# Performance work log

Hardware: AMD Instinct MI355X
Metric: run time of the kernel (lower is better)

## Reference

```python
import jax, jax.numpy as jnp
import numpy as np

DIM = 64
NUM_GRAPHS = 256
SLOPE = 11.0 / 48.0  # RReLU eval slope = ((1/8)+(1/3))/2
EPS = 1e-5


def _bn(x, g, b):
    m = x.mean(0)
    v = x.var(0)  # biased, matches torch BN normalization
    return (x - m) * jax.lax.rsqrt(v + EPS) * g + b


def _rrelu(x):
    return jnp.where(x >= 0, x, SLOPE * x)


def _gru(x, h, Wih, Whh, bih, bhh):
    gi = x @ Wih.T + bih
    gh = h @ Whh.T + bhh
    ir, iz, inn = jnp.split(gi, 3, -1)
    hr, hz, hn = jnp.split(gh, 3, -1)
    r = jax.nn.sigmoid(ir + hr)
    z = jax.nn.sigmoid(iz + hz)
    n = jnp.tanh(inn + r * hn)
    return (1.0 - z) * n + z * h


def _nnconv(x, ei, We, bias, n_nodes):
    # edge-conditioned conv: gather src, per-edge matmul, scatter-mean to dst
    src, dst = ei[0], ei[1]
    msg = jnp.einsum('ei,eio->eo', x[src], We)
    s = jax.ops.segment_sum(msg, dst, num_segments=n_nodes)
    cnt = jax.ops.segment_sum(jnp.ones((ei.shape[1],), x.dtype), dst, num_segments=n_nodes)
    return s / jnp.maximum(cnt, 1.0)[:, None] + bias


def _seg_softmax(e, seg, nseg):
    m = jax.ops.segment_max(e, seg, num_segments=nseg)
    ex = jnp.exp(e - m[seg])
    den = jax.ops.segment_sum(ex, seg, num_segments=nseg)
    return ex / den[seg]


def _set2set(x, seg, nseg, Wih, Whh, bih, bhh, steps=3):
    H = x.shape[-1]
    q_star = jnp.zeros((nseg, 2 * H), x.dtype)
    h = jnp.zeros((nseg, H), x.dtype)
    c = jnp.zeros((nseg, H), x.dtype)
    for _ in range(steps):
        gates = q_star @ Wih.T + bih + h @ Whh.T + bhh
        i, f, g, o = jnp.split(gates, 4, -1)
        c = jax.nn.sigmoid(f) * c + jax.nn.sigmoid(i) * jnp.tanh(g)
        h = jax.nn.sigmoid(o) * jnp.tanh(c)
        e = jnp.sum(x * h[seg], -1)
        a = _seg_softmax(e, seg, nseg)
        r = jax.ops.segment_sum(a[:, None] * x, seg, num_segments=nseg)
        q_star = jnp.concatenate([h, r], -1)
    return q_star


def reference(x, edge_index, edge_attr, edge_index3, edge_attr3, batch,
              bnx_g, bnx_b, Wn, bnode, We, be, Wnn1, bias1,
              Wih1, Whh1, bih1, bhh1, bnc_g, bnc_b, Wc1, bc1, Wc2, bc2,
              Wnn2, bias2, Wih2, Whh2, bih2, bhh2,
              Ws_ih, Ws_hh, bs_ih, bs_hh, bno_g, bno_b, Ww, Wb):
    N = x.shape[0]
    out = _rrelu(_bn(x, bnx_g, bnx_b) @ Wn + bnode)          # [N, 64]
    ea = _rrelu(edge_attr @ We + be)                          # [E, 12]
    W1 = (ea @ Wnn1).reshape(-1, DIM, DIM)                    # [E, 64, 64]
    h = out
    for _ in range(2):
        m = _rrelu(_nnconv(out, edge_index, W1, bias1, N))
        h = _gru(m, h, Wih1, Whh1, bih1, bhh1)
        out = h
    out = _bn(out, bnc_g, bnc_b)
    out = _rrelu(out @ Wc1 + bc1)
    out = _rrelu(out @ Wc2 + bc2)                             # [N, 128] (dropout=identity in eval)
    ei3s = jnp.concatenate([edge_index3, edge_index3[::-1]], axis=1)
    ea3s = jnp.concatenate([edge_attr3, edge_attr3], axis=0)
    W2 = (ea3s @ Wnn2).reshape(-1, 2 * DIM, 2 * DIM)          # [2*E3, 128, 128]
    h = out
    for _ in range(2):
        m = _rrelu(_nnconv(out, ei3s, W2, bias2, N))
        h = _gru(m, h, Wih2, Whh2, bih2, bhh2)
        out = h
    cbi = batch[edge_index3[0]]
    pool = _set2set(out, batch, NUM_GRAPHS, Ws_ih, Ws_hh, bs_ih, bs_hh)[cbi]
    t0 = out[edge_index3[0]]
    t1 = out[edge_index3[1]]
    yhat = jnp.concatenate([(t0 + t1) * 0.5, t0 * t1, (t0 - t1) ** 2, pool], axis=1)  # [E3, 640]
    yhat = _bn(yhat, bno_g, bno_b)
    w = edge_attr3 @ Ww
    b = edge_attr3 @ Wb
    return jnp.sum(yhat * w, axis=1) + b[:, 0]


def setup_inputs() -> dict:
    key = jax.random.key(0)
    ks = iter(jax.random.split(key, 64))
    def nrm(shape, scale=1.0):
        return jax.random.normal(next(ks), shape, jnp.float32) * scale
    def lin(i, o):
        return nrm((i, o), 1.0 / np.sqrt(i))
    N, E, E3 = 8192, 16384, 1024
    inp = {}
    inp['x'] = nrm((N, 8))
    inp['edge_index'] = jax.random.randint(next(ks), (2, E), 0, N)
    inp['edge_attr'] = nrm((E, 19))
    inp['edge_index3'] = jax.random.randint(next(ks), (2, E3), 0, N)
    inp['edge_attr3'] = nrm((E3, 8))
    inp['batch'] = jnp.repeat(jnp.arange(NUM_GRAPHS), N // NUM_GRAPHS)
    inp['bnx_g'] = jnp.ones(8); inp['bnx_b'] = jnp.zeros(8)
    inp['Wn'] = lin(8, 64); inp['bnode'] = jnp.zeros(64)
    inp['We'] = lin(19, 12); inp['be'] = jnp.zeros(12)
    inp['Wnn1'] = lin(12, DIM * DIM) * 0.5; inp['bias1'] = jnp.zeros(64)
    inp['Wih1'] = nrm((192, 64), 1.0 / np.sqrt(64)); inp['Whh1'] = nrm((192, 64), 1.0 / np.sqrt(64))
    inp['bih1'] = jnp.zeros(192); inp['bhh1'] = jnp.zeros(192)
    inp['bnc_g'] = jnp.ones(64); inp['bnc_b'] = jnp.zeros(64)
    inp['Wc1'] = lin(64, 128); inp['bc1'] = jnp.zeros(128)
    inp['Wc2'] = lin(128, 128); inp['bc2'] = jnp.zeros(128)
    inp['Wnn2'] = lin(8, 4 * DIM * DIM) * 0.5; inp['bias2'] = jnp.zeros(128)
    inp['Wih2'] = nrm((384, 128), 1.0 / np.sqrt(128)); inp['Whh2'] = nrm((384, 128), 1.0 / np.sqrt(128))
    inp['bih2'] = jnp.zeros(384); inp['bhh2'] = jnp.zeros(384)
    inp['Ws_ih'] = nrm((512, 256), 1.0 / np.sqrt(256)); inp['Ws_hh'] = nrm((512, 128), 1.0 / np.sqrt(128))
    inp['bs_ih'] = jnp.zeros(512); inp['bs_hh'] = jnp.zeros(512)
    inp['bno_g'] = jnp.ones(640); inp['bno_b'] = jnp.zeros(640)
    inp['Ww'] = lin(8, 640); inp['Wb'] = lin(8, 1)
    return inp
```

## Files before the change

### kernel.cpp

```cpp
#include <hip/hip_runtime.h>
#include <hip/hip_bf16.h>
#include <math.h>

#define N_NODES 8192
#define N_EDGES 16384
#define N_E3    1024
#define NGRAPH  256
#define NPG     32
#define SLOPE   (11.0f/48.0f)
#define BN_EPS  1e-5f

__device__ __forceinline__ float rrelu(float v){ return v >= 0.f ? v : SLOPE*v; }
__device__ __forceinline__ float sigm(float v){ return 1.f/(1.f+__expf(-v)); }

typedef _Float16 f16;
typedef __attribute__((ext_vector_type(8))) _Float16 half8v;
typedef __attribute__((ext_vector_type(4))) float f32x4;

__device__ __forceinline__ void zero_tail(int zb, float* zptr, int zcount) {
  float4 z4 = make_float4(0.f,0.f,0.f,0.f);
  int bd = blockDim.x;
  for (int i = zb*bd + (int)threadIdx.x; i*4 < zcount; i += 16*bd)
    ((float4*)zptr)[i] = z4;
}

__global__ __launch_bounds__(256) void conv1f_k(const float* __restrict__ nodeA,
    const int* __restrict__ ei, const float* __restrict__ ea,
    const f16* __restrict__ Wz1h, float* __restrict__ sbuf) {
  int t = threadIdx.x, lane = t & 63, wv = t >> 6;
  int e0 = blockIdx.x*64 + wv*16;
  int eA = e0 + (lane & 15);
  int src = ei[eA];
  int kb0 = (lane >> 4) * 8;
  const float* ap = nodeA + (size_t)src*64 + kb0;
  float4 v0 = *(const float4*)ap,      v1 = *(const float4*)(ap+4);
  float4 v2 = *(const float4*)(ap+32), v3 = *(const float4*)(ap+36);
  half8v a0, a1;
  a0[0]=(f16)v0.x; a0[1]=(f16)v0.y; a0[2]=(f16)v0.z; a0[3]=(f16)v0.w;
  a0[4]=(f16)v1.x; a0[5]=(f16)v1.y; a0[6]=(f16)v1.z; a0[7]=(f16)v1.w;
  a1[0]=(f16)v2.x; a1[1]=(f16)v2.y; a1[2]=(f16)v2.z; a1[3]=(f16)v2.w;
  a1[4]=(f16)v3.x; a1[5]=(f16)v3.y; a1[6]=(f16)v3.z; a1[7]=(f16)v3.w;
  float eav[12];
  #pragma unroll
  for (int kg = 0; kg < 12; kg++) eav[kg] = ea[eA*12 + kg];

  f32x4 acc[4] = {{0,0,0,0},{0,0,0,0},{0,0,0,0},{0,0,0,0}};
  #pragma unroll
  for (int kg = 0; kg < 12; kg++) {
    f16 s = (f16)eav[kg];
    half8v s0, s1;
    #pragma unroll
    for (int u = 0; u < 8; u++) { s0[u] = a0[u]*s; s1[u] = a1[u]*s; }
    #pragma unroll
    for (int jf = 0; jf < 4; jf++) {
      const f16* wp = Wz1h + (size_t)(kg*64 + jf*16 + (lane & 15))*64 + kb0;
      acc[jf] = __builtin_amdgcn_mfma_f32_16x16x32_f16(s0, *(const half8v*)wp, acc[jf], 0, 0, 0);
      acc[jf] = __builtin_amdgcn_mfma_f32_16x16x32_f16(s1, *(const half8v*)(wp+32), acc[jf], 0, 0, 0);
    }
  }
  int dstv[4];
  #pragma unroll
  for (int r = 0; r < 4; r++) dstv[r] = ei[N_EDGES + e0 + ((lane>>4)<<2) + r];
  #pragma unroll
  for (int jf = 0; jf < 4; jf++) {
    int col = jf*16 + (lane & 15);
    #pragma unroll
    for (int r = 0; r < 4; r++)
      atomicAdd(&sbuf[dstv[r]*64 + col], acc[jf][r]);
  }
}

__global__ __launch_bounds__(512) void conv2f_k(const float* __restrict__ nodeB,
    const int* __restrict__ ei3, const float* __restrict__ ea3,
    const f16* __restrict__ W2fh, float* __restrict__ sbuf) {
  int t = threadIdx.x, lane = t & 63, wv = t >> 6;
  int eg = blockIdx.x >> 1, qh = blockIdx.x & 1;
  int kgh = wv >> 2, jp = wv & 3;
  int e0 = eg * 16;
  int eA = e0 + (lane & 15);
  int src = ei3[eA];
  int kb0 = qh*64 + (lane >> 4) * 8;
  const float* ap = nodeB + (size_t)src*128 + kb0;
  half8v a0, a1;
  {
    float4 w0 = *(const float4*)ap,        w1 = *(const float4*)(ap+4);
    float4 w2 = *(const float4*)(ap + 32), w3 = *(const float4*)(ap+36);
    a0[0]=(f16)w0.x; a0[1]=(f16)w0.y; a0[2]=(f16)w0.z; a0[3]=(f16)w0.w;
    a0[4]=(f16)w1.x; a0[5]=(f16)w1.y; a0[6]=(f16)w1.z; a0[7]=(f16)w1.w;
    a1[0]=(f16)w2.x; a1[1]=(f16)w2.y; a1[2]=(f16)w2.z; a1[3]=(f16)w2.w;
    a1[4]=(f16)w3.x; a1[5]=(f16)w3.y; a1[6]=(f16)w3.z; a1[7]=(f16)w3.w;
  }
  int eb = eA & (N_E3 - 1);
  float eav[4];
  #pragma unroll
  for (int kk = 0; kk < 4; kk++) eav[kk] = ea3[eb*8 + kgh*4 + kk];

  f32x4 acc[2] = {{0,0,0,0},{0,0,0,0}};
  #pragma unroll
  for (int kk = 0; kk < 4; kk++) {
    f16 s = (f16)eav[kk];
    half8v s0, s1;
    #pragma unroll
    for (int u = 0; u < 8; u++) { s0[u] = a0[u]*s; s1[u] = a1[u]*s; }
    int kg = kgh*4 + kk;
    #pragma unroll
    for (int jj = 0; jj < 2; jj++) {
      int jf = jp*2 + jj;
      const f16* wp = W2fh + (size_t)(kg*128 + jf*16 + (lane & 15))*128 + kb0;
      acc[jj] = __builtin_amdgcn_mfma_f32_16x16x32_f16(s0, *(const half8v*)wp, acc[jj], 0, 0, 0);
      acc[jj] = __builtin_amdgcn_mfma_f32_16x16x32_f16(s1, *(const half8v*)(wp+32), acc[jj], 0, 0, 0);
    }
  }
  int dstv[4];
  #pragma unroll
  for (int r = 0; r < 4; r++) dstv[r] = ei3[(e0 + ((lane>>4)<<2) + r + N_E3) & (2*N_E3 - 1)];
  #pragma unroll
  for (int jj = 0; jj < 2; jj++) {
    int col = (jp*2+jj)*16 + (lane & 15);
    #pragma unroll
    for (int r = 0; r < 4; r++)
      atomicAdd(&sbuf[dstv[r]*128 + col], acc[jj][r]);
  }
}

template<int LOGH, int STATS>
__global__ void gruf_k(const float* __restrict__ sbuf, const float* __restrict__ cnt,
                       const float* __restrict__ mbias,
                       const f16* __restrict__ Wih, const f16* __restrict__ Whh,
                       const float* __restrict__ bih, const float* __restrict__ bhh,
                       const float* __restrict__ hold, float* __restrict__ hnew,
                       float* __restrict__ bns1, float* __restrict__ bns2,
                       int nblk, float* __restrict__ zptr, int zcount) {
  if ((int)blockIdx.x >= nblk) { zero_tail(blockIdx.x - nblk, zptr, zcount); return; }
  const int H = 1 << LOGH;
  const int K = H;
  const int jt = H >> 6;
  int t = threadIdx.x;
  int lane = t & 63, wv = t >> 6;
  int wpb = blockDim.x >> 6;
  int bm = blockIdx.x / jt, bj = blockIdx.x % jt;
  int n0 = bm * (wpb << 4) + (wv << 4);
  int j0 = bj << 6;
  int row = n0 + (lane & 15);
  int kb0 = (lane >> 4) * 8;

  f32x4 aR[4]  = {{0,0,0,0},{0,0,0,0},{0,0,0,0},{0,0,0,0}};
  f32x4 aZ[4]  = {{0,0,0,0},{0,0,0,0},{0,0,0,0},{0,0,0,0}};
  f32x4 aIN[4] = {{0,0,0,0},{0,0,0,0},{0,0,0,0},{0,0,0,0}};
  f32x4 aHN[4] = {{0,0,0,0},{0,0,0,0},{0,0,0,0},{0,0,0,0}};

  float dn = 1.f / fmaxf(cnt[row], 1.0f);
  for (int k0 = 0; k0 < K; k0 += 32) {
    int kb = k0 + kb0;
    const float* ap = sbuf + (size_t)row * K + kb;
    float4 v0 = *(const float4*)ap, v1 = *(const float4*)(ap + 4);
    float4 b0 = *(const float4*)(mbias + kb), b1 = *(const float4*)(mbias + kb + 4);
    half8v af;
    af[0]=(f16)rrelu(v0.x*dn+b0.x); af[1]=(f16)rrelu(v0.y*dn+b0.y);
    af[2]=(f16)rrelu(v0.z*dn+b0.z); af[3]=(f16)rrelu(v0.w*dn+b0.w);
    af[4]=(f16)rrelu(v1.x*dn+b1.x); af[5]=(f16)rrelu(v1.y*dn+b1.y);
    af[6]=(f16)rrelu(v1.z*dn+b1.z); af[7]=(f16)rrelu(v1.w*dn+b1.w);
    #pragma unroll
    for (int jf = 0; jf < 4; jf++) {
      int wr = j0 + jf*16 + (lane & 15);
      half8v wR = *(const half8v*)(Wih + (size_t)wr*K + kb);
      half8v wZ = *(const half8v*)(Wih + (size_t)(H + wr)*K + kb);
      half8v wN = *(const half8v*)(Wih + (size_t)(2*H + wr)*K + kb);
      aR[jf]  = __builtin_amdgcn_mfma_f32_16x16x32_f16(af, wR, aR[jf], 0, 0, 0);
      aZ[jf]  = __builtin_amdgcn_mfma_f32_16x16x32_f16(af, wZ, aZ[jf], 0, 0, 0);
      aIN[jf] = __builtin_amdgcn_mfma_f32_16x16x32_f16(af, wN, aIN[jf], 0, 0, 0);
    }
  }
  for (int k0 = 0; k0 < K; k0 += 32) {
    int kb = k0 + kb0;
    const float* ap = hold + (size_t)row * K + kb;
    float4 v0 = *(const float4*)ap, v1 = *(const float4*)(ap + 4);
    half8v af;
    af[0]=(f16)v0.x; af[1]=(f16)v0.y; af[2]=(f16)v0.z; af[3]=(f16)v0.w;
    af[4]=(f16)v1.x; af[5]=(f16)v1.y; af[6]=(f16)v1.z; af[7]=(f16)v1.w;
    #pragma unroll
    for (int jf = 0; jf < 4; jf++) {
      int wr = j0 + jf*16 + (lane & 15);
      half8v wR = *(const half8v*)(Whh + (size_t)wr*K + kb);
      half8v wZ = *(const half8v*)(Whh + (size_t)(H + wr)*K + kb);
      half8v wN = *(const half8v*)(Whh + (size_t)(2*H + wr)*K + kb);
      aR[jf]  = __builtin_amdgcn_mfma_f32_16x16x32_f16(af, wR, aR[jf], 0, 0, 0);
      aZ[jf]  = __builtin_amdgcn_mfma_f32_16x16x32_f16(af, wZ, aZ[jf], 0, 0, 0);
      aHN[jf] = __builtin_amdgcn_mfma_f32_16x16x32_f16(af, wN, aHN[jf], 0, 0, 0);
    }
  }
  int r0 = n0 + ((lane >> 4) << 2);
  #pragma unroll
  for (int jf = 0; jf < 4; jf++) {
    int col = j0 + jf*16 + (lane & 15);
    float bR = bih[col] + bhh[col];
    float bZ = bih[H + col] + bhh[H + col];
    float bI = bih[2*H + col], bH = bhh[2*H + col];
    float ssum = 0.f, sq = 0.f;
    #pragma unroll
    for (int r = 0; r < 4; r++) {
      float rr = sigm(aR[jf][r] + bR);
      float zz = sigm(aZ[jf][r] + bZ);
      float nn = tanhf(aIN[jf][r] + bI + rr*(aHN[jf][r] + bH));
      float ho = hold[(size_t)(r0 + r)*H + col];
      float hv = (1.f - zz)*nn + zz*ho;
      hnew[(size_t)(r0 + r)*H + col] = hv;
      if (STATS) { ssum += hv; sq += hv*hv; }
    }
    if (STATS) {
      ssum += __shfl_xor(ssum, 16); ssum += __shfl_xor(ssum, 32);
      sq   += __shfl_xor(sq, 16);   sq   += __shfl_xor(sq, 32);
      if (lane < 16) { atomicAdd(&bns1[col], ssum); atomicAdd(&bns2[col], sq); }
    }
  }
}

__global__ __launch_bounds__(256) void fcf_k(const float* __restrict__ A,
    const f16* __restrict__ W1, const float* __restrict__ b1v,
    const f16* __restrict__ W2, const float* __restrict__ b2v,
    const float* __restrict__ bns1, const float* __restrict__ bns2,
    const float* __restrict__ g, const float* __restrict__ b,
    float* __restrict__ outB,
    int nblk, float* __restrict__ zptr, int zcount) {
  if ((int)blockIdx.x >= nblk) { zero_tail(blockIdx.x - nblk, zptr, zcount); return; }
  __shared__ f16 y1s[4][16][128];
  int t = threadIdx.x, lane = t & 63, wv = t >> 6;
  int n0 = blockIdx.x*64 + wv*16;
  int row = n0 + (lane & 15);
  int kb0 = (lane >> 4) * 8;
  const float invN = 1.f / (float)N_NODES;

  const float* ap = A + (size_t)row*64 + kb0;
  half8v af0, af1;
  #pragma unroll
  for (int u = 0; u < 8; u++) {
    int k0i = kb0 + u, k1i = 32 + kb0 + u;
    float m0 = bns1[k0i]*invN, m1 = bns1[k1i]*invN;
    float va0 = bns2[k0i]*invN - m0*m0, va1 = bns2[k1i]*invN - m1*m1;
    af0[u] = (f16)((ap[u]    - m0)*rsqrtf(va0+BN_EPS)*g[k0i] + b[k0i]);
    af1[u] = (f16)((ap[32+u] - m1)*rsqrtf(va1+BN_EPS)*g[k1i] + b[k1i]);
  }
  f32x4 acc1[8] = {{0,0,0,0},{0,0,0,0},{0,0,0,0},{0,0,0,0},
                   {0,0,0,0},{0,0,0,0},{0,0,0,0},{0,0,0,0}};
  #pragma unroll
  for (int jf = 0; jf < 8; jf++) {
    const f16* wp = W1 + (size_t)(jf*16 + (lane & 15))*64 + kb0;
    acc1[jf] = __builtin_amdgcn_mfma_f32_16x16x32_f16(af0, *(const half8v*)wp, acc1[jf], 0, 0, 0);
    acc1[jf] = __builtin_amdgcn_mfma_f32_16x16x32_f16(af1, *(const half8v*)(wp+32), acc1[jf], 0, 0, 0);
  }
  #pragma unroll
  for (int jf = 0; jf < 8; jf++) {
    int col = jf*16 + (lane & 15);
    float bv = b1v[col];
    #pragma unroll
    for (int r = 0; r < 4; r++) {
      int rl = ((lane >> 4) << 2) + r;
      y1s[wv][rl][col] = (f16)rrelu(acc1[jf][r] + bv);
    }
  }
  __syncthreads();
  half8v bf[4];
  #pragma unroll
  for (int q = 0; q < 4; q++)
    bf[q] = *(const half8v*)&y1s[wv][lane & 15][q*32 + kb0];
  f32x4 acc2[8] = {{0,0,0,0},{0,0,0,0},{0,0,0,0},{0,0,0,0},
                   {0,0,0,0},{0,0,0,0},{0,0,0,0},{0,0,0,0}};
  #pragma unroll
  for (int jf = 0; jf < 8; jf++) {
    const f16* wp = W2 + (size_t)(jf*16 + (lane & 15))*128 + kb0;
    #pragma unroll
    for (int q = 0; q < 4; q++)
      acc2[jf] = __builtin_amdgcn_mfma_f32_16x16x32_f16(bf[q], *(const half8v*)(wp + q*32), acc2[jf], 0, 0, 0);
  }
  int r0 = n0 + ((lane >> 4) << 2);
  #pragma unroll
  for (int jf = 0; jf < 8; jf++) {
    int col = jf*16 + (lane & 15);
    float bv = b2v[col];
    #pragma unroll
    for (int r = 0; r < 4; r++)
      outB[(size_t)(r0 + r)*128 + col] = rrelu(acc2[jf][r] + bv);
  }
}

__global__ void embed_k(const float* __restrict__ x,
                        const float* __restrict__ mean, const float* __restrict__ var,
                        const float* __restrict__ g, const float* __restrict__ b,
                        const float* __restrict__ Wn, const float* __restrict__ bnode,
                        float* __restrict__ nodeA,
                        const float* __restrict__ eattr,
                        const float* __restrict__ We, const float* __restrict__ be,
                        float* __restrict__ ea12,
                        const int* __restrict__ ei, const int* __restrict__ ei3,
                        float* __restrict__ cnt1, float* __restrict__ cnt2,
                        float* __restrict__ zptr) {
  int bid = blockIdx.x, t = threadIdx.x;
  if (bid < 2048) {
    int idx = bid * 256 + t;
    int n = idx >> 6, o = idx & 63;
    float acc = bnode[o];
    #pragma unroll
    for (int i = 0; i < 8; i++) {
      float xn = (x[n*8+i] - mean[i]) * rsqrtf(var[i] + BN_EPS) * g[i] + b[i];
      acc += xn * Wn[i*64 + o];
    }
    nodeA[idx] = rrelu(acc);
  } else if (bid < 2816) {
    int idx = (bid - 2048) * 256 + t;
    if (idx >= N_EDGES * 12) return;
    int e = idx / 12, j = idx - e * 12;
    float acc = be[j];
    #pragma unroll
    for (int k = 0; k < 19; k++) acc += eattr[e*19+k] * We[k*12 + j];
    ea12[idx] = rrelu(acc);
  } else if (bid < 2880) {
    int idx = (bid - 2816) * 256 + t;
    if (idx < N_EDGES) atomicAdd(&cnt1[ei[N_EDGES + idx]], 1.0f);
    if (idx < N_E3) {
      atomicAdd(&cnt2[ei3[N_E3 + idx]], 1.0f);
      atomicAdd(&cnt2[ei3[idx]], 1.0f);
    }
  } else {
    zero_tail(bid - 2880, zptr, N_NODES*64);
  }
}

__global__ void pack_k(const float* __restrict__ Wnn1,
                       const float* __restrict__ Wih1, const float* __restrict__ Whh1,
                       const float* __restrict__ Wc1,  const float* __restrict__ Wc2,
                       const float* __restrict__ Wnn2,
                       const float* __restrict__ Wih2, const float* __restrict__ Whh2,
                       const float* __restrict__ Ws_ih, const float* __restrict__ Ws_hh,
                       const float* __restrict__ x,
                       f16* __restrict__ Wz1h,
                       f16* __restrict__ Wih1h, f16* __restrict__ Whh1h,
                       f16* __restrict__ Wc1Th, f16* __restrict__ Wc2Th,
                       f16* __restrict__ W2fh,
                       f16* __restrict__ Wih2h, f16* __restrict__ Whh2h,
                       float* __restrict__ Wfold,
                       float* __restrict__ cnt1, float* __restrict__ cnt2,
                       float* __restrict__ bns1, float* __restrict__ bns2,
                       float* __restrict__ mean, float* __restrict__ var) {
  if (blockIdx.x >= 512) {
    int f = blockIdx.x - 512, t = threadIdx.x;
    __shared__ float s1[256], s2[256];
    float a = 0.f, bq = 0.f;
    for (int n = t; n < N_NODES; n += 256) {
      float v = x[n*8 + f];
      a += v; bq += v*v;
    }
    s1[t] = a; s2[t] = bq; __syncthreads();
    for (int w = 128; w > 0; w >>= 1) {
      if (t < w) { s1[t] += s1[t+w]; s2[t] += s2[t+w]; }
      __syncthreads();
    }
    if (t == 0) {
      float m = s1[0] / (float)N_NODES;
      mean[f] = m;
      var[f]  = s2[0] / (float)N_NODES - m*m;
    }
    return;
  }
  int idx = blockIdx.x * 256 + threadIdx.x;
  if (idx < 49152) {
    int jj = idx >> 6, i = idx & 63;
    int k = jj >> 6, o = jj & 63;
    Wz1h[idx] = (f16)Wnn1[k*4096 + i*64 + o];
  }
  if (idx < 12288) { Wih1h[idx] = (f16)Wih1[idx]; Whh1h[idx] = (f16)Whh1[idx]; }
  if (idx < 8192) {
    int o = idx >> 6, i = idx & 63;
    Wc1Th[idx] = (f16)Wc1[i*128 + o];
  }
  if (idx < 16384) {
    int o = idx >> 7, i = idx & 127;
    Wc2Th[idx] = (f16)Wc2[i*128 + o];
  }
  if (idx < 131072) {
    int r = idx >> 7, i = idx & 127;
    int k = r >> 7, o = r & 127;
    W2fh[idx] = (f16)Wnn2[k*16384 + i*128 + o];
  }
  if (idx < 49152) { Wih2h[idx] = (f16)Wih2[idx]; Whh2h[idx] = (f16)Whh2[idx]; }
  if (idx < 131072) {
    int i = idx >> 9, j = idx & 511;
    float v = Ws_ih[(size_t)j*256 + i];
    if (i < 128) v += Ws_hh[(size_t)j*128 + i];
    Wfold[idx] = v;
  }
  if (idx < N_NODES) { cnt1[idx] = 0.f; cnt2[idx] = 0.f; }
  if (idx < 128) { bns1[idx] = 0.f; bns2[idx] = 0.f; }
}

__global__ __launch_bounds__(1024) void set2set_k(const float* __restrict__ x,
    const float* __restrict__ Wfold,
    const float* __restrict__ bs_ih, const float* __restrict__ bs_hh,
    float* __restrict__ qpool) {
  int g = blockIdx.x, t = threadIdx.x;
  __shared__ float xs[NPG*128];
  __shared__ float hr[256];
  __shared__ float cbuf[128];
  __shared__ float pbuf[1024];
  __shared__ float abuf[NPG];
  *(float4*)&xs[t*4] = *(const float4*)(x + (size_t)g*NPG*128 + t*4);
  if (t < 128) {
    float gi = bs_ih[t]     + bs_hh[t];
    float gg = bs_ih[256+t] + bs_hh[256+t];
    float go = bs_ih[384+t] + bs_hh[384+t];
    float c0 = sigm(gi) * tanhf(gg);
    cbuf[t] = c0;
    hr[t] = sigm(go) * tanhf(c0);
  }
  __syncthreads();
  #pragma unroll 1
  for (int step = 0; step < 3; step++) {
    {
      int node = t >> 5, s = t & 31;
      const float* xr = xs + node*128 + s*4;
      float pv = xr[0]*hr[s*4] + xr[1]*hr[s*4+1] + xr[2]*hr[s*4+2] + xr[3]*hr[s*4+3];
      pv += __shfl_down(pv, 16, 32); pv += __shfl_down(pv, 8, 32);
      pv += __shfl_down(pv, 4, 32);  pv += __shfl_down(pv, 2, 32);
      pv += __shfl_down(pv, 1, 32);
      if (s == 0) pbuf[node] = pv;
    }
    __syncthreads();
    if (t < NPG) {
      float e = pbuf[t];
      float mx = e;
      for (int o = 16; o > 0; o >>= 1) mx = fmaxf(mx, __shfl_xor(mx, o, 32));
      float ex = __expf(e - mx);
      float den = ex;
      for (int o = 16; o > 0; o >>= 1) den += __shfl_xor(den, o, 32);
      abuf[t] = ex / den;
    }
    __syncthreads();
    if (t < 128) {
      float r = 0.f;
      #pragma unroll 8
      for (int nn = 0; nn < NPG; nn++) r += abuf[nn] * xs[nn*128 + t];
      hr[128 + t] = r;
    }
    __syncthreads();
    if (step == 2) break;
    {
      int j = t & 511, half = t >> 9;
      const float* wp = Wfold + (size_t)(half*128)*512 + j;
      const float* iv = hr + half*128;
      float a0=0.f, a1=0.f, a2=0.f, a3=0.f;
      #pragma unroll 4
      for (int i = 0; i < 128; i += 4) {
        a0 += iv[i]   * wp[(i)  *512];
        a1 += iv[i+1] * wp[(i+1)*512];
        a2 += iv[i+2] * wp[(i+2)*512];
        a3 += iv[i+3] * wp[(i+3)*512];
      }
      pbuf[t] = a0 + a1 + a2 + a3;
    }
    __syncthreads();
    if (t < 128) {
      float gi = pbuf[t]     + pbuf[512+t] + bs_ih[t]     + bs_hh[t];
      float gf = pbuf[128+t] + pbuf[640+t] + bs_ih[128+t] + bs_hh[128+t];
      float gg = pbuf[256+t] + pbuf[768+t] + bs_ih[256+t] + bs_hh[256+t];
      float go = pbuf[384+t] + pbuf[896+t] + bs_ih[384+t] + bs_hh[384+t];
      float ci = sigm(gf) * cbuf[t] + sigm(gi) * tanhf(gg);
      cbuf[t] = ci;
      hr[t] = sigm(go) * tanhf(ci);
    }
    __syncthreads();
  }
  if (t < 256) qpool[g*256 + t] = hr[t];
}

__global__ __launch_bounds__(256) void ys_k(const float* __restrict__ feat,
    const int* __restrict__ ei3, const int* __restrict__ batch,
    const float* __restrict__ qpool,
    float* __restrict__ yhat, float* __restrict__ mean, float* __restrict__ var) {
  int t = threadIdx.x, lane = t & 63, wv = t >> 6;
  int j = blockIdx.x*4 + wv;
  float s = 0.f, q = 0.f;
  for (int e = lane; e < N_E3; e += 64) {
    int s0 = ei3[e], s1 = ei3[N_E3 + e];
    float v;
    if (j < 128)      { v = 0.5f * (feat[s0*128+j] + feat[s1*128+j]); }
    else if (j < 256) { int jj = j-128; v = feat[s0*128+jj] * feat[s1*128+jj]; }
    else if (j < 384) { int jj = j-256; float d = feat[s0*128+jj] - feat[s1*128+jj]; v = d*d; }
    else              { int cbi = batch[s0]; v = qpool[cbi*256 + (j-384)]; }
    yhat[(size_t)e*640 + j] = v;
    s += v; q += v*v;
  }
  #pragma unroll
  for (int o = 32; o > 0; o >>= 1) { s += __shfl_xor(s, o); q += __shfl_xor(q, o); }
  if (lane == 0) {
    float m = s / (float)N_E3;
    mean[j] = m;
    var[j]  = q / (float)N_E3 - m*m;
  }
}

__global__ void final_k(const float* __restrict__ yhat,
                        const float* __restrict__ mean, const float* __restrict__ var,
                        const float* __restrict__ g, const float* __restrict__ b,
                        const float* __restrict__ ea3,
                        const float* __restrict__ Ww, const float* __restrict__ Wb,
                        float* __restrict__ out) {
  int e = blockIdx.x, t = threadIdx.x;
  __shared__ float red[128];
  float av[8];
  #pragma unroll
  for (int k = 0; k < 8; k++) av[k] = ea3[e*8 + k];
  float acc = 0.f;
  for (int j = t; j < 640; j += 128) {
    float yn = (yhat[(size_t)e*640 + j] - mean[j]) * rsqrtf(var[j] + BN_EPS) * g[j] + b[j];
    float wj = 0.f;
    #pragma unroll
    for (int k = 0; k < 8; k++) wj += av[k] * Ww[k*640 + j];
    acc += yn * wj;
  }
  red[t] = acc; __syncthreads();
  for (int w = 64; w > 0; w >>= 1) {
    if (t < w) red[t] += red[t+w];
    __syncthreads();
  }
  if (t == 0) {
    float bb = 0.f;
    #pragma unroll
    for (int k = 0; k < 8; k++) bb += av[k] * Wb[k];
    out[e] = red[0] + bb;
  }
}

extern "C" void kernel_launch(void* const* d_in, const int* in_sizes, int n_in,
                              void* d_out, int out_size, void* d_ws, size_t ws_size,
                              hipStream_t stream) {
  const float* x      = (const float*)d_in[0];
  const int*   ei     = (const int*)  d_in[1];
  const float* eattr  = (const float*)d_in[2];
  const int*   ei3    = (const int*)  d_in[3];
  const float* ea3    = (const float*)d_in[4];
  const int*   batch  = (const int*)  d_in[5];
  const float* bnx_g  = (const float*)d_in[6];
  const float* bnx_b  = (const float*)d_in[7];
  const float* Wn     = (const float*)d_in[8];
  const float* bnode  = (const float*)d_in[9];
  const float* We     = (const float*)d_in[10];
  const float* be     = (const float*)d_in[11];
  const float* Wnn1   = (const float*)d_in[12];
  const float* bias1  = (const float*)d_in[13];
  const float* Wih1   = (const float*)d_in[14];
  const float* Whh1   = (const float*)d_in[15];
  const float* bih1   = (const float*)d_in[16];
  const float* bhh1   = (const float*)d_in[17];
  const float* bnc_g  = (const float*)d_in[18];
  const float* bnc_b  = (const float*)d_in[19];
  const float* Wc1    = (const float*)d_in[20];
  const float* bc1    = (const float*)d_in[21];
  const float* Wc2    = (const float*)d_in[22];
  const float* bc2    = (const float*)d_in[23];
  const float* Wnn2   = (const float*)d_in[24];
  const float* bias2  = (const float*)d_in[25];
  const float* Wih2   = (const float*)d_in[26];
  const float* Whh2   = (const float*)d_in[27];
  const float* bih2   = (const float*)d_in[28];
  const float* bhh2   = (const float*)d_in[29];
  const float* Ws_ih  = (const float*)d_in[30];
  const float* Ws_hh  = (const float*)d_in[31];
  const float* bs_ih  = (const float*)d_in[32];
  const float* bs_hh  = (const float*)d_in[33];
  const float* bno_g  = (const float*)d_in[34];
  const float* bno_b  = (const float*)d_in[35];
  const float* Ww     = (const float*)d_in[36];
  const float* Wb     = (const float*)d_in[37];
  float* out = (float*)d_out;

  float* W = (float*)d_ws;
  size_t off = 0;
  float* Wfold  = W + off; off += 131072;
  float* ea12   = W + off; off += (size_t)N_EDGES * 12;
  float* nodeA  = W + off; off += (size_t)N_NODES * 64;
  float* nodeA2 = W + off; off += (size_t)N_NODES * 64;
  float* sA1    = W + off; off += (size_t)N_NODES * 64;
  float* sA2    = W + off; off += (size_t)N_NODES * 64;
  float* sB1    = W + off; off += (size_t)N_NODES * 128;
  float* sB2    = W + off; off += (size_t)N_NODES * 128;
  float* cnt1   = W + off; off += (size_t)N_NODES;
  float* cnt2   = W + off; off += (size_t)N_NODES;
  float* nodeB  = W + off; off += (size_t)N_NODES * 128;
  float* nodeB2 = W + off; off += (size_t)N_NODES * 128;
  float* qpool  = W + off; off += (size_t)NGRAPH * 256;
  float* yhat   = W + off; off += (size_t)N_E3 * 640;
  float* mean   = W + off; off += 640;
  float* var    = W + off; off += 640;
  float* bns1   = W + off; off += 128;
  float* bns2   = W + off; off += 128;
  f16* F = (f16*)(W + off);
  size_t foff = 0;
  f16* Wz1h  = F + foff; foff += 49152;
  f16* Wih1h = F + foff; foff += 12288;
  f16* Whh1h = F + foff; foff += 12288;
  f16* Wc1Th = F + foff; foff += 8192;
  f16* Wc2Th = F + foff; foff += 16384;
  f16* W2fh  = F + foff; foff += 131072;
  f16* Wih2h = F + foff; foff += 49152;
  f16* Whh2h = F + foff; foff += 49152;
  (void)foff; (void)ws_size; (void)in_sizes; (void)n_in; (void)out_size;

  pack_k<<<520, 256, 0, stream>>>(Wnn1, Wih1, Whh1, Wc1, Wc2, Wnn2, Wih2, Whh2, Ws_ih, Ws_hh, x,
                                  Wz1h, Wih1h, Whh1h, Wc1Th, Wc2Th, W2fh, Wih2h, Whh2h,
                                  Wfold, cnt1, cnt2, bns1, bns2, mean, var);
  embed_k<<<2896, 256, 0, stream>>>(x, mean, var, bnx_g, bnx_b, Wn, bnode, nodeA,
                                    eattr, We, be, ea12, ei, ei3, cnt1, cnt2, sA1);

  conv1f_k<<<256, 256, 0, stream>>>(nodeA, ei, ea12, Wz1h, sA1);
  gruf_k<6,0><<<272, 128, 0, stream>>>(sA1, cnt1, bias1, Wih1h, Whh1h, bih1, bhh1,
                                       nodeA, nodeA2, nullptr, nullptr,
                                       256, sA2, N_NODES*64);
  conv1f_k<<<256, 256, 0, stream>>>(nodeA2, ei, ea12, Wz1h, sA2);
  gruf_k<6,1><<<272, 128, 0, stream>>>(sA2, cnt1, bias1, Wih1h, Whh1h, bih1, bhh1,
                                       nodeA2, nodeA, bns1, bns2,
                                       256, sB1, N_NODES*128);

  fcf_k<<<144, 256, 0, stream>>>(nodeA, Wc1Th, bc1, Wc2Th, bc2,
                                 bns1, bns2, bnc_g, bnc_b, nodeB,
                                 128, sB2, N_NODES*128);

  conv2f_k<<<256, 512, 0, stream>>>(nodeB, ei3, ea3, W2fh, sB1);
  gruf_k<7,0><<<256, 256, 0, stream>>>(sB1, cnt2, bias2, Wih2h, Whh2h, bih2, bhh2,
                                       nodeB, nodeB2, nullptr, nullptr,
                                       256, nullptr, 0);
  conv2f_k<<<256, 512, 0, stream>>>(nodeB2, ei3, ea3, W2fh, sB2);
  gruf_k<7,0><<<256, 256, 0, stream>>>(sB2, cnt2, bias2, Wih2h, Whh2h, bih2, bhh2,
                                       nodeB2, nodeB, nullptr, nullptr,
                                       256, nullptr, 0);

  set2set_k<<<NGRAPH, 1024, 0, stream>>>(nodeB, Wfold, bs_ih, bs_hh, qpool);

  ys_k<<<160, 256, 0, stream>>>(nodeB, ei3, batch, qpool, yhat, mean, var);

  final_k<<<N_E3, 128, 0, stream>>>(yhat, mean, var, bno_g, bno_b, ea3, Ww, Wb, out);
}
```

Baseline: 201.1 us.

## Tile-transpose weight packing via shared memory and coalesce ys_k edge-major with atomics

The weight-pack kernel now transposes Wnn2, Ws_ih/Ws_hh, Wnn1, Wc1 and Wc2 through a padded 64x65 shared-memory tile, so both reads and writes are coalesced and fewer blocks are launched. ys_k is restructured so that each block handles 8 edges, with threads spanning the 640 feature columns. This makes the feat gathers and yhat stores coalesced. Column sums and sums of squares are accumulated with atomics into zeroed buffers, and final_k derives the mean and variance from them. The atomic accumulation adds contention and makes float summation order nondeterministic.

```diff
diff --git a/kernel.cpp b/kernel.cpp
--- a/kernel.cpp
+++ b/kernel.cpp
@@ -325,7 +325,7 @@
   }
 }
 
-__global__ void pack_k(const float* __restrict__ Wnn1,
+__global__ __launch_bounds__(256) void pack_k(const float* __restrict__ Wnn1,
                        const float* __restrict__ Wih1, const float* __restrict__ Whh1,
                        const float* __restrict__ Wc1,  const float* __restrict__ Wc2,
                        const float* __restrict__ Wnn2,
@@ -340,9 +340,23 @@
                        float* __restrict__ Wfold,
                        float* __restrict__ cnt1, float* __restrict__ cnt2,
                        float* __restrict__ bns1, float* __restrict__ bns2,
+                       float* __restrict__ ysum, float* __restrict__ ysq,
                        float* __restrict__ mean, float* __restrict__ var) {
-  if (blockIdx.x >= 512) {
-    int f = blockIdx.x - 512, t = threadIdx.x;
+  __shared__ float tile[64][65];
+  int bid = blockIdx.x, t = threadIdx.x;
+  int col = t & 63, rq = t >> 6;
+
+  if (bid < 192) {
+    int idx = bid * 256 + t;
+    if (idx < 49152) { Wih2h[idx] = (f16)Wih2[idx]; Whh2h[idx] = (f16)Whh2[idx]; }
+    if (idx < 12288) { Wih1h[idx] = (f16)Wih1[idx]; Whh1h[idx] = (f16)Whh1[idx]; }
+    if (idx < N_NODES) { cnt1[idx] = 0.f; cnt2[idx] = 0.f; }
+    if (idx < 128) { bns1[idx] = 0.f; bns2[idx] = 0.f; }
+    if (idx < 640) { ysum[idx] = 0.f; ysq[idx] = 0.f; }
+    return;
+  }
+  if (bid >= 274) {
+    int f = bid - 274;
     __shared__ float s1[256], s2[256];
     float a = 0.f, bq = 0.f;
     for (int n = t; n < N_NODES; n += 256) {
@@ -361,35 +375,55 @@
     }
     return;
   }
-  int idx = blockIdx.x * 256 + threadIdx.x;
-  if (idx < 49152) {
-    int jj = idx >> 6, i = idx & 63;
-    int k = jj >> 6, o = jj & 63;
-    Wz1h[idx] = (f16)Wnn1[k*4096 + i*64 + o];
-  }
-  if (idx < 12288) { Wih1h[idx] = (f16)Wih1[idx]; Whh1h[idx] = (f16)Whh1[idx]; }
-  if (idx < 8192) {
-    int o = idx >> 6, i = idx & 63;
-    Wc1Th[idx] = (f16)Wc1[i*128 + o];
-  }
-  if (idx < 16384) {
-    int o = idx >> 7, i = idx & 127;
-    Wc2Th[idx] = (f16)Wc2[i*128 + o];
-  }
-  if (idx < 131072) {
-    int r = idx >> 7, i = idx & 127;
-    int k = r >> 7, o = r & 127;
-    W2fh[idx] = (f16)Wnn2[k*16384 + i*128 + o];
-  }
-  if (idx < 49152) { Wih2h[idx] = (f16)Wih2[idx]; Whh2h[idx] = (f16)Whh2[idx]; }
-  if (idx < 131072) {
-    int i = idx >> 9, j = idx & 511;
-    float v = Ws_ih[(size_t)j*256 + i];
-    if (i < 128) v += Ws_hh[(size_t)j*128 + i];
-    Wfold[idx] = v;
-  }
-  if (idx < N_NODES) { cnt1[idx] = 0.f; cnt2[idx] = 0.f; }
-  if (idx < 128) { bns1[idx] = 0.f; bns2[idx] = 0.f; }
+
+  const float *srcA = nullptr, *srcB = nullptr;
+  int sAs = 0, sBs = 0, dsts = 0;
+  f16* dstH = nullptr; float* dstF = nullptr;
+
+  if (bid < 224) {
+    int tt = bid - 192, kg = tt >> 2, ti = (tt >> 1) & 1, tj = tt & 1;
+    srcA = Wnn2 + kg*16384 + (ti*64)*128 + tj*64;  sAs = 128;
+    dstH = W2fh + kg*16384 + (tj*64)*128 + ti*64;  dsts = 128;
+  } else if (bid < 256) {
+    int tt = bid - 224, bi = tt >> 3, bj = tt & 7;
+    srcA = Ws_ih + (size_t)(bj*64)*256 + bi*64;  sAs = 256;
+    if (bi*64 < 128) { srcB = Ws_hh + (size_t)(bj*64)*128 + bi*64; sBs = 128; }
+    dstF = Wfold + (size_t)(bi*64)*512 + bj*64;  dsts = 512;
+  } else if (bid < 268) {
+    int kg = bid - 256;
+    srcA = Wnn1 + kg*4096;  sAs = 64;
+    dstH = Wz1h + kg*4096;  dsts = 64;
+  } else if (bid < 270) {
+    int to = bid - 268;
+    srcA = Wc1 + to*64;          sAs = 128;
+    dstH = Wc1Th + (to*64)*64;   dsts = 64;
+  } else {
+    int tt = bid - 270, ti = tt >> 1, to = tt & 1;
+    srcA = Wc2 + (ti*64)*128 + to*64;          sAs = 128;
+    dstH = Wc2Th + (to*64)*128 + ti*64;        dsts = 128;
+  }
+
+  #pragma unroll
+  for (int p = 0; p < 16; p++) {
+    int r = p*4 + rq;
+    float v = srcA[(size_t)r*sAs + col];
+    if (srcB) v += srcB[(size_t)r*sBs + col];
+    tile[r][col] = v;
+  }
+  __syncthreads();
+  if (dstH) {
+    #pragma unroll
+    for (int p = 0; p < 16; p++) {
+      int c = p*4 + rq;
+      dstH[(size_t)c*dsts + col] = (f16)tile[col][c];
+    }
+  } else {
+    #pragma unroll
+    for (int p = 0; p < 16; p++) {
+      int c = p*4 + rq;
+      dstF[(size_t)c*dsts + col] = tile[col][c];
+    }
+  }
 }
 
 __global__ __launch_bounds__(1024) void set2set_k(const float* __restrict__ x,
@@ -471,46 +505,57 @@
   if (t < 256) qpool[g*256 + t] = hr[t];
 }
 
+__device__ __forceinline__ float yval(const float* __restrict__ feat,
+                                      const float* __restrict__ qpool,
+                                      int n0, int n1, int cb, int j) {
+  if (j < 128)      return 0.5f*(feat[n0*128+j] + feat[n1*128+j]);
+  else if (j < 256) { int jj=j-128; return feat[n0*128+jj]*feat[n1*128+jj]; }
+  else if (j < 384) { int jj=j-256; float d=feat[n0*128+jj]-feat[n1*128+jj]; return d*d; }
+  else              return qpool[cb*256 + (j-384)];
+}
+
 __global__ __launch_bounds__(256) void ys_k(const float* __restrict__ feat,
     const int* __restrict__ ei3, const int* __restrict__ batch,
     const float* __restrict__ qpool,
-    float* __restrict__ yhat, float* __restrict__ mean, float* __restrict__ var) {
-  int t = threadIdx.x, lane = t & 63, wv = t >> 6;
-  int j = blockIdx.x*4 + wv;
-  float s = 0.f, q = 0.f;
-  for (int e = lane; e < N_E3; e += 64) {
-    int s0 = ei3[e], s1 = ei3[N_E3 + e];
-    float v;
-    if (j < 128)      { v = 0.5f * (feat[s0*128+j] + feat[s1*128+j]); }
-    else if (j < 256) { int jj = j-128; v = feat[s0*128+jj] * feat[s1*128+jj]; }
-    else if (j < 384) { int jj = j-256; float d = feat[s0*128+jj] - feat[s1*128+jj]; v = d*d; }
-    else              { int cbi = batch[s0]; v = qpool[cbi*256 + (j-384)]; }
-    yhat[(size_t)e*640 + j] = v;
-    s += v; q += v*v;
-  }
-  #pragma unroll
-  for (int o = 32; o > 0; o >>= 1) { s += __shfl_xor(s, o); q += __shfl_xor(q, o); }
-  if (lane == 0) {
-    float m = s / (float)N_E3;
-    mean[j] = m;
-    var[j]  = q / (float)N_E3 - m*m;
-  }
+    float* __restrict__ yhat, float* __restrict__ ysum, float* __restrict__ ysq) {
+  int t = threadIdx.x;
+  int e0 = blockIdx.x * 8;
+  float s0=0,q0=0,s1=0,q1=0,s2=0,q2=0;
+  for (int ee = 0; ee < 8; ee++) {
+    int e = e0 + ee;
+    int n0 = ei3[e], n1 = ei3[N_E3 + e];
+    int cb = batch[n0];
+    float v0 = yval(feat, qpool, n0, n1, cb, t);
+    yhat[(size_t)e*640 + t] = v0; s0 += v0; q0 += v0*v0;
+    float v1 = yval(feat, qpool, n0, n1, cb, t + 256);
+    yhat[(size_t)e*640 + t + 256] = v1; s1 += v1; q1 += v1*v1;
+    if (t < 128) {
+      float v2 = yval(feat, qpool, n0, n1, cb, t + 512);
+      yhat[(size_t)e*640 + t + 512] = v2; s2 += v2; q2 += v2*v2;
+    }
+  }
+  atomicAdd(&ysum[t], s0);        atomicAdd(&ysq[t], q0);
+  atomicAdd(&ysum[t + 256], s1);  atomicAdd(&ysq[t + 256], q1);
+  if (t < 128) { atomicAdd(&ysum[t + 512], s2); atomicAdd(&ysq[t + 512], q2); }
 }
 
 __global__ void final_k(const float* __restrict__ yhat,
-                        const float* __restrict__ mean, const float* __restrict__ var,
+                        const float* __restrict__ ysum, const float* __restrict__ ysq,
                         const float* __restrict__ g, const float* __restrict__ b,
                         const float* __restrict__ ea3,
                         const float* __restrict__ Ww, const float* __restrict__ Wb,
                         float* __restrict__ out) {
   int e = blockIdx.x, t = threadIdx.x;
   __shared__ float red[128];
+  const float invE = 1.f / (float)N_E3;
   float av[8];
   #pragma unroll
   for (int k = 0; k < 8; k++) av[k] = ea3[e*8 + k];
   float acc = 0.f;
   for (int j = t; j < 640; j += 128) {
-    float yn = (yhat[(size_t)e*640 + j] - mean[j]) * rsqrtf(var[j] + BN_EPS) * g[j] + b[j];
+    float m = ysum[j] * invE;
+    float v = ysq[j] * invE - m*m;
+    float yn = (yhat[(size_t)e*640 + j] - m) * rsqrtf(v + BN_EPS) * g[j] + b[j];
     float wj = 0.f;
     #pragma unroll
     for (int k = 0; k < 8; k++) wj += av[k] * Ww[k*640 + j];
@@ -592,6 +637,8 @@
   float* var    = W + off; off += 640;
   float* bns1   = W + off; off += 128;
   float* bns2   = W + off; off += 128;
+  float* ysum   = W + off; off += 640;
+  float* ysq    = W + off; off += 640;
   f16* F = (f16*)(W + off);
   size_t foff = 0;
   f16* Wz1h  = F + foff; foff += 49152;
@@ -604,9 +651,9 @@
   f16* Whh2h = F + foff; foff += 49152;
   (void)foff; (void)ws_size; (void)in_sizes; (void)n_in; (void)out_size;
 
-  pack_k<<<520, 256, 0, stream>>>(Wnn1, Wih1, Whh1, Wc1, Wc2, Wnn2, Wih2, Whh2, Ws_ih, Ws_hh, x,
+  pack_k<<<282, 256, 0, stream>>>(Wnn1, Wih1, Whh1, Wc1, Wc2, Wnn2, Wih2, Whh2, Ws_ih, Ws_hh, x,
                                   Wz1h, Wih1h, Whh1h, Wc1Th, Wc2Th, W2fh, Wih2h, Whh2h,
-                                  Wfold, cnt1, cnt2, bns1, bns2, mean, var);
+                                  Wfold, cnt1, cnt2, bns1, bns2, ysum, ysq, mean, var);
   embed_k<<<2896, 256, 0, stream>>>(x, mean, var, bnx_g, bnx_b, Wn, bnode, nodeA,
                                     eattr, We, be, ea12, ei, ei3, cnt1, cnt2, sA1);
 
@@ -634,7 +681,7 @@
 
   set2set_k<<<NGRAPH, 1024, 0, stream>>>(nodeB, Wfold, bs_ih, bs_hh, qpool);
 
-  ys_k<<<160, 256, 0, stream>>>(nodeB, ei3, batch, qpool, yhat, mean, var);
-
-  final_k<<<N_E3, 128, 0, stream>>>(yhat, mean, var, bno_g, bno_b, ea3, Ww, Wb, out);
-}
+  ys_k<<<128, 256, 0, stream>>>(nodeB, ei3, batch, qpool, yhat, ysum, ysq);
+
+  final_k<<<N_E3, 128, 0, stream>>>(yhat, ysum, ysq, bno_g, bno_b, ea3, Ww, Wb, out);
+}
```

Result: faster. 196.6 us (-2.2%).
